# Optimization experiments

Hardware: AMD Instinct MI355X
Metric: run time of the kernel (lower is better)

## Reference

```python
import jax, jax.numpy as jnp
import numpy as np
import math

B, S, D, H = 2, 2048, 1024, 16
DH = D // H
MASK_VALUE = -1000000.0  # module uses -1e6, not -inf


def setup_inputs() -> dict:
    key = jax.random.key(0)
    ks = jax.random.split(key, 8)
    scale = 1.0 / math.sqrt(D)
    return {
        "queries": jax.random.normal(ks[0], (B, S, D), jnp.float32),
        "keys": jax.random.normal(ks[1], (B, S, D), jnp.float32),
        "values": jax.random.normal(ks[2], (B, S, D), jnp.float32),
        "valid_lens": jax.random.randint(ks[3], (B,), 1, S + 1, jnp.int32),
        "Wq": jax.random.normal(ks[4], (D, D), jnp.float32) * scale,
        "Wk": jax.random.normal(ks[5], (D, D), jnp.float32) * scale,
        "Wv": jax.random.normal(ks[6], (D, D), jnp.float32) * scale,
        "Wo": jax.random.normal(ks[7], (D, D), jnp.float32) * scale,
    }


def _split_heads(x):
    # [B, S, D] -> [B, H, S, DH]
    b, s, d = x.shape
    return x.reshape(b, s, H, DH).transpose(0, 2, 1, 3)


def reference(queries, keys, values, valid_lens, Wq, Wk, Wv, Wo):
    q = _split_heads(queries @ Wq)          # [B, H, S, DH]
    k = _split_heads(keys @ Wk)
    v = _split_heads(values @ Wv)
    scores = jnp.einsum("bhqd,bhkd->bhqk", q, k) / math.sqrt(DH)
    # valid_lens [B]: one length per batch row, broadcast over heads & queries
    mask = jnp.arange(scores.shape[-1])[None, None, None, :] < valid_lens[:, None, None, None]
    scores = jnp.where(mask, scores, MASK_VALUE)
    attn = jax.nn.softmax(scores, axis=-1)  # dropout is identity in eval
    out = jnp.einsum("bhqk,bhkd->bhqd", attn, v)   # [B, H, S, DH]
    out = out.transpose(0, 2, 1, 3).reshape(queries.shape[0], queries.shape[1], D)
    return out @ Wo
```

## Files before the change

kernel.cpp:

```cpp
#include <hip/hip_runtime.h>
#include <stdint.h>

#define BB 2
#define SS 2048
#define DD 1024
#define HH 16
#define DHD 64
#define MM (BB * SS)

typedef unsigned short u16;
typedef unsigned int u32;
typedef __attribute__((ext_vector_type(8))) short bhalf8;
typedef __attribute__((ext_vector_type(4))) float floatx4;
typedef __attribute__((ext_vector_type(2))) u32 u32x2;
typedef __attribute__((address_space(3))) u32 as3_u32;
typedef __attribute__((address_space(1))) u32 as1_u32;

__device__ __forceinline__ u16 f2bf(float f) {
  u32 u = __float_as_uint(f);
  u32 r = (u + 0x7FFFu + ((u >> 16) & 1u)) >> 16;
  return (u16)r;
}

__device__ __forceinline__ u32 cvtpk_bf16(float lo, float hi) {
  u32 r;
  asm("v_cvt_pk_bf16_f32 %0, %1, %2" : "=v"(r) : "v"(lo), "v"(hi));
  return r;
}

__device__ __forceinline__ float exp2_fast(float x) {
  float r;
  asm("v_exp_f32 %0, %1" : "=v"(r) : "v"(x));
  return r;
}

__device__ __forceinline__ void gload16(const void* g, const void* l) {
  __builtin_amdgcn_global_load_lds((as1_u32*)(uintptr_t)g, (as3_u32*)(uintptr_t)l, 16, 0, 0);
}

__global__ void k_convert3(const float* __restrict__ q, const float* __restrict__ k,
                           const float* __restrict__ v, u16* __restrict__ out) {
  const int z = blockIdx.y;
  const float* src = (z == 0) ? q : (z == 1) ? k : v;
  const int i = blockIdx.x * 256 + threadIdx.x;
  float4 val = ((const float4*)src)[i];
  ushort4 o;
  o.x = f2bf(val.x); o.y = f2bf(val.y); o.z = f2bf(val.z); o.w = f2bf(val.w);
  ((ushort4*)(out + (size_t)z * 4194304))[i] = o;
}

__global__ void k_transpose4(const float* __restrict__ Wq, const float* __restrict__ Wk,
                             const float* __restrict__ Wv, const float* __restrict__ Wo,
                             u16* __restrict__ Wt) {
  const int z = blockIdx.z;
  const float* W = (z == 0) ? Wq : (z == 1) ? Wk : (z == 2) ? Wv : Wo;
  const float sc = (z == 0) ? 0.18033688011112042f : 1.0f;
  __shared__ u16 tile[32][33];
  const int tx = threadIdx.x, ty = threadIdx.y;
  const int n0 = blockIdx.x * 32, k0 = blockIdx.y * 32;
#pragma unroll
  for (int i = 0; i < 4; ++i)
    tile[ty + 8 * i][tx] = f2bf(W[(size_t)(k0 + ty + 8 * i) * DD + n0 + tx] * sc);
  __syncthreads();
  u16* dst = Wt + (size_t)z * 1048576;
#pragma unroll
  for (int i = 0; i < 4; ++i)
    dst[(size_t)(n0 + ty + 8 * i) * DD + k0 + tx] = tile[tx][ty + 8 * i];
}

__global__ __launch_bounds__(256, 2) void k_gemm_qkv(
    const u16* __restrict__ Xq, const u16* __restrict__ Xk, const u16* __restrict__ Xv,
    const u16* __restrict__ Wt, u16* __restrict__ Qb, u16* __restrict__ Kb,
    u16* __restrict__ Vtb) {
  const int z = blockIdx.z;
  const u16* A = (z == 0) ? Xq : (z == 1) ? Xk : Xv;
  const u16* Bt = Wt + (size_t)z * 1048576;
  __shared__ __attribute__((aligned(16))) u16 sA[2][128 * 32];
  __shared__ __attribute__((aligned(16))) u16 sB[2][128 * 32];
  const int t = threadIdx.x;
  const int w = t >> 6, lane = t & 63;
  const int lr = lane & 15, lg = lane >> 4;
  const int wr = w >> 1, wc = w & 1;
  const int row0 = blockIdx.y * 128, col0 = blockIdx.x * 128;

  const int srow = t >> 2;
  const int skoff = (t & 3) * 8;
  const u16* gA = A + (size_t)(row0 + srow) * DD + skoff;
  const u16* gB = Bt + (size_t)(col0 + srow) * DD + skoff;
  const int ldsbase = w * 512;

  floatx4 acc[4][4] = {};

  auto stage = [&](int buf, int kt) {
    const int ko = kt * 32;
    gload16(gA + ko, &sA[buf][ldsbase]);
    gload16(gA + ko + (size_t)64 * DD, &sA[buf][2048 + ldsbase]);
    gload16(gB + ko, &sB[buf][ldsbase]);
    gload16(gB + ko + (size_t)64 * DD, &sB[buf][2048 + ldsbase]);
  };

  int cur = 0;
  stage(0, 0);
  __syncthreads();
  for (int kt = 0; kt < 32; ++kt) {
    if (kt + 1 < 32) stage(cur ^ 1, kt + 1);
    bhalf8 af[4], bf[4];
#pragma unroll
    for (int m = 0; m < 4; ++m)
      af[m] = *(const bhalf8*)&sA[cur][(wr * 64 + m * 16 + lr) * 32 + lg * 8];
#pragma unroll
    for (int n = 0; n < 4; ++n)
      bf[n] = *(const bhalf8*)&sB[cur][(wc * 64 + n * 16 + lr) * 32 + lg * 8];
#pragma unroll
    for (int m = 0; m < 4; ++m)
#pragma unroll
      for (int n = 0; n < 4; ++n)
        acc[m][n] = __builtin_amdgcn_mfma_f32_16x16x32_bf16(af[m], bf[n], acc[m][n], 0, 0, 0);
    __syncthreads();
    cur ^= 1;
  }

#pragma unroll
  for (int m = 0; m < 4; ++m) {
#pragma unroll
    for (int n = 0; n < 4; ++n) {
      const int col = col0 + wc * 64 + n * 16 + lr;
      const int rowb = row0 + wr * 64 + m * 16 + lg * 4;
      if (z == 2) {
        const int bidx = rowb >> 11, s = rowb & (SS - 1);
        ushort4 pk;
        pk.x = f2bf(acc[m][n][0]); pk.y = f2bf(acc[m][n][1]);
        pk.z = f2bf(acc[m][n][2]); pk.w = f2bf(acc[m][n][3]);
        *(ushort4*)&Vtb[((size_t)bidx * 1024 + col) * SS + s] = pk;
      } else {
        u16* C = (z == 0) ? Qb : Kb;
#pragma unroll
        for (int r = 0; r < 4; ++r)
          C[(size_t)(rowb + r) * DD + col] = f2bf(acc[m][n][r]);
      }
    }
  }
}

__global__ __launch_bounds__(256, 2) void k_gemm_wo(
    const u16* __restrict__ A, const u16* __restrict__ Bt, float* __restrict__ C) {
  __shared__ __attribute__((aligned(16))) u16 sA[2][64 * 32];
  __shared__ __attribute__((aligned(16))) u16 sB[2][128 * 32];
  const int t = threadIdx.x;
  const int w = t >> 6, lane = t & 63;
  const int lr = lane & 15, lg = lane >> 4;
  const int wr = w >> 1, wc = w & 1;
  const int row0 = blockIdx.y * 64, col0 = blockIdx.x * 128;

  const int srow = t >> 2;
  const int skoff = (t & 3) * 8;
  const u16* gA = A + (size_t)(row0 + srow) * DD + skoff;
  const u16* gB = Bt + (size_t)(col0 + srow) * DD + skoff;
  const int ldsbase = w * 512;

  floatx4 acc[2][4] = {};

  auto stage = [&](int buf, int kt) {
    const int ko = kt * 32;
    gload16(gA + ko, &sA[buf][ldsbase]);
    gload16(gB + ko, &sB[buf][ldsbase]);
    gload16(gB + ko + (size_t)64 * DD, &sB[buf][2048 + ldsbase]);
  };

  int cur = 0;
  stage(0, 0);
  __syncthreads();
  for (int kt = 0; kt < 32; ++kt) {
    if (kt + 1 < 32) stage(cur ^ 1, kt + 1);
    bhalf8 af[2], bf[4];
#pragma unroll
    for (int m = 0; m < 2; ++m)
      af[m] = *(const bhalf8*)&sA[cur][(wr * 32 + m * 16 + lr) * 32 + lg * 8];
#pragma unroll
    for (int n = 0; n < 4; ++n)
      bf[n] = *(const bhalf8*)&sB[cur][(wc * 64 + n * 16 + lr) * 32 + lg * 8];
#pragma unroll
    for (int m = 0; m < 2; ++m)
#pragma unroll
      for (int n = 0; n < 4; ++n)
        acc[m][n] = __builtin_amdgcn_mfma_f32_16x16x32_bf16(af[m], bf[n], acc[m][n], 0, 0, 0);
    __syncthreads();
    cur ^= 1;
  }

#pragma unroll
  for (int m = 0; m < 2; ++m)
#pragma unroll
    for (int n = 0; n < 4; ++n) {
      const int col = col0 + wc * 64 + n * 16 + lr;
      const int rowb = row0 + wr * 32 + m * 16 + lg * 4;
#pragma unroll
      for (int r = 0; r < 4; ++r)
        C[(size_t)(rowb + r) * DD + col] = acc[m][n][r];
    }
}

__global__ __launch_bounds__(256, 2) void k_attn(
    const u16* __restrict__ Q, const u16* __restrict__ K, const u16* __restrict__ Vt,
    float* __restrict__ Opart, float2* __restrict__ Ml,
    const int* __restrict__ valid_lens, const int part) {
  const int t = threadIdx.x;
  const int w = t >> 6, lane = t & 63;
  const int lr = lane & 15, lg = lane >> 4;
  const int h = blockIdx.y, z = blockIdx.z;
  const int b = z & 1, p = z >> 1;
  const int q0 = blockIdx.x * 64 + w * 16;
  const int vl = valid_lens[b];
  const int kbeg = p * part;
  if (kbeg >= vl) return;
  const int kend = (vl < kbeg + part) ? vl : (kbeg + part);
  const int L = kend - kbeg;

  __shared__ __attribute__((aligned(16))) u16 kbuf[2][64 * 64];
  __shared__ __attribute__((aligned(16))) u16 vbuf[2][64 * 64];
  __shared__ __attribute__((aligned(16))) u16 p_lds[4][16 * 72];
  u16* pl = &p_lds[w][0];

  const u16* Qp = Q + ((size_t)(b * SS + q0 + lr)) * DD + h * DHD;
  const bhalf8 qf0 = *(const bhalf8*)(Qp + lg * 8);
  const bhalf8 qf1 = *(const bhalf8*)(Qp + 32 + lg * 8);

  const int sub = lane >> 3;
  const int sc16 = (lane & 7) ^ sub;
  const u16* ksrc = K + (size_t)(b * SS + kbeg + w * 16 + sub) * DD + h * DHD + sc16 * 8;
  const u16* vsrc = Vt + ((size_t)(b * HH + h) * DHD + w * 16 + sub) * SS + kbeg + sc16 * 8;

  auto stage = [&](int buf, int i) {
    const int sk0 = i * 64;
    gload16(ksrc + (size_t)sk0 * DD,       &kbuf[buf][(w * 16) * 64]);
    gload16(ksrc + (size_t)(sk0 + 8) * DD, &kbuf[buf][(w * 16 + 8) * 64]);
    gload16(vsrc + sk0,                    &vbuf[buf][(w * 16) * 64]);
    gload16(vsrc + (size_t)8 * SS + sk0,   &vbuf[buf][(w * 16 + 8) * 64]);
  };

  float mrun = -1e30f, lrun = 0.f;
  floatx4 o[4] = {};

  const int nblk = (L + 63) >> 6;
  const bool partial = (L & 63) != 0;
  const int swz = lr & 7;

  stage(0, 0);
  __syncthreads();

  int cb = 0;
  for (int i = 0; i < nblk; ++i) {
    if (i + 1 < nblk) stage(cb ^ 1, i + 1);
    const u16* kb = &kbuf[cb][0];
    const u16* vb = &vbuf[cb][0];
    floatx4 s[4];
    __builtin_amdgcn_s_setprio(1);
#pragma unroll
    for (int c = 0; c < 4; ++c) {
      const bhalf8 kc0 = *(const bhalf8*)&kb[(c * 16 + lr) * 64 + ((lg ^ swz) * 8)];
      const bhalf8 kc1 = *(const bhalf8*)&kb[(c * 16 + lr) * 64 + (((lg + 4) ^ swz) * 8)];
      floatx4 zz = {0.f, 0.f, 0.f, 0.f};
      zz = __builtin_amdgcn_mfma_f32_16x16x32_bf16(kc0, qf0, zz, 0, 0, 0);
      s[c] = __builtin_amdgcn_mfma_f32_16x16x32_bf16(kc1, qf1, zz, 0, 0, 0);
    }
    __builtin_amdgcn_s_setprio(0);
    if (partial && i == nblk - 1) {
      const int sk0 = i * 64;
#pragma unroll
      for (int c = 0; c < 4; ++c)
#pragma unroll
        for (int r = 0; r < 4; ++r)
          if (sk0 + c * 16 + lg * 4 + r >= L) s[c][r] = -1e6f;
    }
    float tmax = fmaxf(fmaxf(fmaxf(s[0][0], s[0][1]), fmaxf(s[0][2], s[0][3])),
                       fmaxf(fmaxf(s[1][0], s[1][1]), fmaxf(s[1][2], s[1][3])));
    tmax = fmaxf(tmax, fmaxf(fmaxf(fmaxf(s[2][0], s[2][1]), fmaxf(s[2][2], s[2][3])),
                             fmaxf(fmaxf(s[3][0], s[3][1]), fmaxf(s[3][2], s[3][3]))));
    tmax = fmaxf(tmax, __shfl_xor(tmax, 16));
    tmax = fmaxf(tmax, __shfl_xor(tmax, 32));
    if (!__all(tmax <= mrun + 8.0f)) {
      const float nm = fmaxf(mrun, tmax);
      const float sc = exp2_fast(mrun - nm);
      mrun = nm;
      lrun *= sc;
      float scb[4];
#pragma unroll
      for (int r = 0; r < 4; ++r) scb[r] = __shfl(sc, lg * 4 + r);
#pragma unroll
      for (int dt = 0; dt < 4; ++dt)
#pragma unroll
        for (int r = 0; r < 4; ++r) o[dt][r] *= scb[r];
    }
    float rs = 0.f;
    u32 pk[4][2];
#pragma unroll
    for (int c = 0; c < 4; ++c) {
      float p0 = exp2_fast(s[c][0] - mrun), p1 = exp2_fast(s[c][1] - mrun);
      float p2 = exp2_fast(s[c][2] - mrun), p3 = exp2_fast(s[c][3] - mrun);
      rs += (p0 + p1) + (p2 + p3);
      pk[c][0] = cvtpk_bf16(p0, p1);
      pk[c][1] = cvtpk_bf16(p2, p3);
    }
    rs += __shfl_xor(rs, 16);
    rs += __shfl_xor(rs, 32);
    lrun += rs;
#pragma unroll
    for (int c = 0; c < 4; ++c) {
      u32x2 pr; pr.x = pk[c][0]; pr.y = pk[c][1];
      *(u32x2*)&pl[lr * 72 + c * 16 + lg * 4] = pr;
    }
    asm volatile("s_waitcnt lgkmcnt(0)" ::: "memory");
    const bhalf8 pa0 = *(const bhalf8*)&pl[lr * 72 + lg * 8];
    const bhalf8 pa1 = *(const bhalf8*)&pl[lr * 72 + 32 + lg * 8];
    __builtin_amdgcn_s_setprio(1);
#pragma unroll
    for (int dt = 0; dt < 4; ++dt) {
      const bhalf8 vf0 = *(const bhalf8*)&vb[(dt * 16 + lr) * 64 + ((lg ^ swz) * 8)];
      const bhalf8 vf1 = *(const bhalf8*)&vb[(dt * 16 + lr) * 64 + (((lg + 4) ^ swz) * 8)];
      o[dt] = __builtin_amdgcn_mfma_f32_16x16x32_bf16(pa0, vf0, o[dt], 0, 0, 0);
      o[dt] = __builtin_amdgcn_mfma_f32_16x16x32_bf16(pa1, vf1, o[dt], 0, 0, 0);
    }
    __builtin_amdgcn_s_setprio(0);
    __syncthreads();
    cb ^= 1;
  }

  const size_t rowbase = ((size_t)(b * HH + h)) * SS + q0;
  const size_t pbase = (size_t)p * (BB * HH * SS);
#pragma unroll
  for (int dt = 0; dt < 4; ++dt)
#pragma unroll
    for (int r = 0; r < 4; ++r)
      Opart[(pbase + rowbase + lg * 4 + r) * DHD + dt * 16 + lr] = o[dt][r];
  if (lane < 16) {
    float2 ml; ml.x = mrun; ml.y = lrun;
    Ml[pbase + rowbase + lr] = ml;
  }
}

template <int P>
__global__ void k_merge(const float* __restrict__ Opart, const float2* __restrict__ Ml,
                        const int* __restrict__ valid_lens, u16* __restrict__ Ob) {
  const int t = threadIdx.x;
  const int rid = blockIdx.x * 16 + (t >> 4);
  const int dc = t & 15;
  const int b = rid >> 15;
  const int h = (rid >> 11) & (HH - 1);
  const int s = rid & (SS - 1);
  const int vl = valid_lens[b];
  constexpr int part = SS / P;
  float m[P], l[P];
  float4 o4[P];
  bool live[P];
  float M = -1e30f;
#pragma unroll
  for (int p = 0; p < P; ++p) {
    live[p] = (p * part < vl);
    if (live[p]) {
      float2 ml = Ml[(size_t)p * (BB * HH * SS) + rid];
      m[p] = ml.x; l[p] = ml.y;
      o4[p] = *(const float4*)&Opart[((size_t)p * (BB * HH * SS) + rid) * DHD + dc * 4];
      M = fmaxf(M, m[p]);
    }
  }
  float L = 0.f;
  float4 acc = {0.f, 0.f, 0.f, 0.f};
#pragma unroll
  for (int p = 0; p < P; ++p)
    if (live[p]) {
      const float wgt = exp2_fast(m[p] - M);
      L += l[p] * wgt;
      acc.x += wgt * o4[p].x; acc.y += wgt * o4[p].y;
      acc.z += wgt * o4[p].z; acc.w += wgt * o4[p].w;
    }
  const float inv = 1.0f / L;
  ushort4 r;
  r.x = f2bf(acc.x * inv); r.y = f2bf(acc.y * inv);
  r.z = f2bf(acc.z * inv); r.w = f2bf(acc.w * inv);
  *(ushort4*)&Ob[((size_t)(b * SS + s)) * DD + h * DHD + dc * 4] = r;
}

extern "C" void kernel_launch(void* const* d_in, const int* in_sizes, int n_in,
                              void* d_out, int out_size, void* d_ws, size_t ws_size,
                              hipStream_t stream) {
  const float* q = (const float*)d_in[0];
  const float* k = (const float*)d_in[1];
  const float* v = (const float*)d_in[2];
  const int* vl = (const int*)d_in[3];
  const float* Wq = (const float*)d_in[4];
  const float* Wk = (const float*)d_in[5];
  const float* Wv = (const float*)d_in[6];
  const float* Wo = (const float*)d_in[7];

  char* ws = (char*)d_ws;
  u16* Xq  = (u16*)(ws + 0);
  u16* Wtq = (u16*)(ws + 25165824);
  u16* Wto = (u16*)(ws + 31457280);
  u16* Qb  = (u16*)(ws + 33554432);
  u16* Kb  = (u16*)(ws + 41943040);
  u16* Vtb = (u16*)(ws + 50331648);
  u16* Ob  = (u16*)(ws + 58720256);

  const bool big = ws_size >= (size_t)134 * 1024 * 1024;
  const int P = big ? 4 : 1;
  const int part = SS / P;
  float* Opart = big ? (float*)(ws + 67108864) : (float*)(ws + 0);
  float2* Ml   = big ? (float2*)(ws + 67108864 + (size_t)4 * BB * HH * SS * DHD * 4)
                     : (float2*)(ws + 16777216);

  k_convert3<<<dim3(4096, 3), 256, 0, stream>>>(q, k, v, Xq);
  k_transpose4<<<dim3(32, 32, 4), dim3(32, 8), 0, stream>>>(Wq, Wk, Wv, Wo, Wtq);
  k_gemm_qkv<<<dim3(8, 32, 3), 256, 0, stream>>>(Xq, Xq + 4194304, Xq + 8388608,
                                                 Wtq, Qb, Kb, Vtb);
  k_attn<<<dim3(32, 16, 2 * P), 256, 0, stream>>>(Qb, Kb, Vtb, Opart, Ml, vl, part);
  if (big) k_merge<4><<<4096, 256, 0, stream>>>(Opart, Ml, vl, Ob);
  else     k_merge<1><<<4096, 256, 0, stream>>>(Opart, Ml, vl, Ob);
  k_gemm_wo<<<dim3(8, 64), 256, 0, stream>>>(Ob, Wto, (float*)d_out);
}
```

Before: 217.1 us.

## Remap block indices for XCD-aware L2 locality and halve attention key split

Replaces the 3D grids of the QKV GEMM, attention and output GEMM with 1D grids whose block IDs are remapped so that groups of eight consecutive IDs, which round-robin across the chiplets, share the same weight tile or head. The aim is better L2 reuse per chiplet. The attention split-K factor also drops from 4 to 2, so there are fewer partial outputs to write and merge. The cost is less parallelism in attention when valid lengths are long.

```diff
diff --git a/kernel.cpp b/kernel.cpp
--- a/kernel.cpp
+++ b/kernel.cpp
@@ -72,7 +72,10 @@
     const u16* __restrict__ Xq, const u16* __restrict__ Xk, const u16* __restrict__ Xv,
     const u16* __restrict__ Wt, u16* __restrict__ Qb, u16* __restrict__ Kb,
     u16* __restrict__ Vtb) {
-  const int z = blockIdx.z;
+  const int id = blockIdx.x;
+  const int rr = id & 7, t8 = id >> 3;
+  const int g = (t8 >> 3) * 8 + rr, c = t8 & 7;
+  const int z = g / 32, by = g % 32, bx = c;
   const u16* A = (z == 0) ? Xq : (z == 1) ? Xk : Xv;
   const u16* Bt = Wt + (size_t)z * 1048576;
   __shared__ __attribute__((aligned(16))) u16 sA[2][128 * 32];
@@ -81,7 +84,7 @@
   const int w = t >> 6, lane = t & 63;
   const int lr = lane & 15, lg = lane >> 4;
   const int wr = w >> 1, wc = w & 1;
-  const int row0 = blockIdx.y * 128, col0 = blockIdx.x * 128;
+  const int row0 = by * 128, col0 = bx * 128;
 
   const int srow = t >> 2;
   const int skoff = (t & 3) * 8;
@@ -144,13 +147,17 @@
 
 __global__ __launch_bounds__(256, 2) void k_gemm_wo(
     const u16* __restrict__ A, const u16* __restrict__ Bt, float* __restrict__ C) {
+  const int id = blockIdx.x;
+  const int rr = id & 7, t8 = id >> 3;
+  const int g = (t8 >> 3) * 8 + rr, c = t8 & 7;
+  const int by = g, bx = c;
   __shared__ __attribute__((aligned(16))) u16 sA[2][64 * 32];
   __shared__ __attribute__((aligned(16))) u16 sB[2][128 * 32];
   const int t = threadIdx.x;
   const int w = t >> 6, lane = t & 63;
   const int lr = lane & 15, lg = lane >> 4;
   const int wr = w >> 1, wc = w & 1;
-  const int row0 = blockIdx.y * 64, col0 = blockIdx.x * 128;
+  const int row0 = by * 64, col0 = bx * 128;
 
   const int srow = t >> 2;
   const int skoff = (t & 3) * 8;
@@ -204,12 +211,15 @@
     const u16* __restrict__ Q, const u16* __restrict__ K, const u16* __restrict__ Vt,
     float* __restrict__ Opart, float2* __restrict__ Ml,
     const int* __restrict__ valid_lens, const int part) {
+  const int id = blockIdx.x;
+  const int rr = id & 7, tt = id >> 3;
+  const int g = (tt >> 5) * 8 + rr, c = tt & 31;
+  const int h = g & 15, zi = g >> 4;
+  const int b = zi & 1, p = zi >> 1;
   const int t = threadIdx.x;
   const int w = t >> 6, lane = t & 63;
   const int lr = lane & 15, lg = lane >> 4;
-  const int h = blockIdx.y, z = blockIdx.z;
-  const int b = z & 1, p = z >> 1;
-  const int q0 = blockIdx.x * 64 + w * 16;
+  const int q0 = c * 64 + w * 16;
   const int vl = valid_lens[b];
   const int kbeg = p * part;
   if (kbeg >= vl) return;
@@ -256,21 +266,21 @@
     floatx4 s[4];
     __builtin_amdgcn_s_setprio(1);
 #pragma unroll
-    for (int c = 0; c < 4; ++c) {
-      const bhalf8 kc0 = *(const bhalf8*)&kb[(c * 16 + lr) * 64 + ((lg ^ swz) * 8)];
-      const bhalf8 kc1 = *(const bhalf8*)&kb[(c * 16 + lr) * 64 + (((lg + 4) ^ swz) * 8)];
+    for (int cc = 0; cc < 4; ++cc) {
+      const bhalf8 kc0 = *(const bhalf8*)&kb[(cc * 16 + lr) * 64 + ((lg ^ swz) * 8)];
+      const bhalf8 kc1 = *(const bhalf8*)&kb[(cc * 16 + lr) * 64 + (((lg + 4) ^ swz) * 8)];
       floatx4 zz = {0.f, 0.f, 0.f, 0.f};
       zz = __builtin_amdgcn_mfma_f32_16x16x32_bf16(kc0, qf0, zz, 0, 0, 0);
-      s[c] = __builtin_amdgcn_mfma_f32_16x16x32_bf16(kc1, qf1, zz, 0, 0, 0);
+      s[cc] = __builtin_amdgcn_mfma_f32_16x16x32_bf16(kc1, qf1, zz, 0, 0, 0);
     }
     __builtin_amdgcn_s_setprio(0);
     if (partial && i == nblk - 1) {
       const int sk0 = i * 64;
 #pragma unroll
-      for (int c = 0; c < 4; ++c)
+      for (int cc = 0; cc < 4; ++cc)
 #pragma unroll
         for (int r = 0; r < 4; ++r)
-          if (sk0 + c * 16 + lg * 4 + r >= L) s[c][r] = -1e6f;
+          if (sk0 + cc * 16 + lg * 4 + r >= L) s[cc][r] = -1e6f;
     }
     float tmax = fmaxf(fmaxf(fmaxf(s[0][0], s[0][1]), fmaxf(s[0][2], s[0][3])),
                        fmaxf(fmaxf(s[1][0], s[1][1]), fmaxf(s[1][2], s[1][3])));
@@ -294,20 +304,20 @@
     float rs = 0.f;
     u32 pk[4][2];
 #pragma unroll
-    for (int c = 0; c < 4; ++c) {
-      float p0 = exp2_fast(s[c][0] - mrun), p1 = exp2_fast(s[c][1] - mrun);
-      float p2 = exp2_fast(s[c][2] - mrun), p3 = exp2_fast(s[c][3] - mrun);
+    for (int cc = 0; cc < 4; ++cc) {
+      float p0 = exp2_fast(s[cc][0] - mrun), p1 = exp2_fast(s[cc][1] - mrun);
+      float p2 = exp2_fast(s[cc][2] - mrun), p3 = exp2_fast(s[cc][3] - mrun);
       rs += (p0 + p1) + (p2 + p3);
-      pk[c][0] = cvtpk_bf16(p0, p1);
-      pk[c][1] = cvtpk_bf16(p2, p3);
+      pk[cc][0] = cvtpk_bf16(p0, p1);
+      pk[cc][1] = cvtpk_bf16(p2, p3);
     }
     rs += __shfl_xor(rs, 16);
     rs += __shfl_xor(rs, 32);
     lrun += rs;
 #pragma unroll
-    for (int c = 0; c < 4; ++c) {
-      u32x2 pr; pr.x = pk[c][0]; pr.y = pk[c][1];
-      *(u32x2*)&pl[lr * 72 + c * 16 + lg * 4] = pr;
+    for (int cc = 0; cc < 4; ++cc) {
+      u32x2 pr; pr.x = pk[cc][0]; pr.y = pk[cc][1];
+      *(u32x2*)&pl[lr * 72 + cc * 16 + lg * 4] = pr;
     }
     asm volatile("s_waitcnt lgkmcnt(0)" ::: "memory");
     const bhalf8 pa0 = *(const bhalf8*)&pl[lr * 72 + lg * 8];
@@ -402,18 +412,17 @@
   u16* Ob  = (u16*)(ws + 58720256);
 
   const bool big = ws_size >= (size_t)134 * 1024 * 1024;
-  const int P = big ? 4 : 1;
+  const int P = big ? 2 : 1;
   const int part = SS / P;
   float* Opart = big ? (float*)(ws + 67108864) : (float*)(ws + 0);
-  float2* Ml   = big ? (float2*)(ws + 67108864 + (size_t)4 * BB * HH * SS * DHD * 4)
+  float2* Ml   = big ? (float2*)(ws + 67108864 + (size_t)2 * BB * HH * SS * DHD * 4)
                      : (float2*)(ws + 16777216);
 
   k_convert3<<<dim3(4096, 3), 256, 0, stream>>>(q, k, v, Xq);
   k_transpose4<<<dim3(32, 32, 4), dim3(32, 8), 0, stream>>>(Wq, Wk, Wv, Wo, Wtq);
-  k_gemm_qkv<<<dim3(8, 32, 3), 256, 0, stream>>>(Xq, Xq + 4194304, Xq + 8388608,
-                                                 Wtq, Qb, Kb, Vtb);
-  k_attn<<<dim3(32, 16, 2 * P), 256, 0, stream>>>(Qb, Kb, Vtb, Opart, Ml, vl, part);
-  if (big) k_merge<4><<<4096, 256, 0, stream>>>(Opart, Ml, vl, Ob);
+  k_gemm_qkv<<<768, 256, 0, stream>>>(Xq, Xq + 4194304, Xq + 8388608, Wtq, Qb, Kb, Vtb);
+  k_attn<<<1024 * P, 256, 0, stream>>>(Qb, Kb, Vtb, Opart, Ml, vl, part);
+  if (big) k_merge<2><<<4096, 256, 0, stream>>>(Opart, Ml, vl, Ob);
   else     k_merge<1><<<4096, 256, 0, stream>>>(Opart, Ml, vl, Ob);
-  k_gemm_wo<<<dim3(8, 64), 256, 0, stream>>>(Ob, Wto, (float*)d_out);
-}
+  k_gemm_wo<<<512, 256, 0, stream>>>(Ob, Wto, (float*)d_out);
+}
```

After: 205.5 us. 5.3% less time.
